# Kernel optimization log

Hardware: AMD Instinct MI355X
Metric: run time of the kernel (lower is better)

Reference implementation:

```python
import jax, jax.numpy as jnp
import numpy as np

B, S, D, H = 8, 1300, 1080, 12
DK = D // H  # 90
FF = 3 * D   # 3240
EPS = 1e-5


def _layernorm(x, g, b):
    m = jnp.mean(x, axis=-1, keepdims=True)
    v = jnp.var(x, axis=-1, keepdims=True)
    return (x - m) * jax.lax.rsqrt(v + EPS) * g + b


def _rotate_half(x):
    x1, x2 = jnp.split(x, 2, axis=-1)
    return jnp.concatenate([-x2, x1], axis=-1)


def _rope(x, cos, sin):
    # x: [B,H,S,DK]; cos/sin: [S,DK] broadcast over batch/heads
    return x * cos + _rotate_half(x) * sin


def setup_inputs() -> dict:
    key = jax.random.key(0)
    ks = jax.random.split(key, 20)
    w = lambda k, sh: jax.random.normal(k, sh, dtype=jnp.float32) * 0.02
    inp = {
        'x': jax.random.normal(ks[0], (B, S, D), dtype=jnp.float32),
        'mask': jnp.tril(jnp.ones((S, S), dtype=jnp.int32))[None, None, :, :],
        'Wq': w(ks[1], (D, D)), 'bq': jnp.zeros((D,), jnp.float32),
        'Wk': w(ks[2], (D, D)), 'bk': jnp.zeros((D,), jnp.float32),
        'Wv': w(ks[3], (D, D)), 'bv': jnp.zeros((D,), jnp.float32),
        'Wo': w(ks[4], (D, D)), 'bo': jnp.zeros((D,), jnp.float32),
        'W1': w(ks[5], (D, FF)), 'b1': jnp.zeros((FF,), jnp.float32),
        'W2': w(ks[6], (FF, D)), 'b2': jnp.zeros((D,), jnp.float32),
        'W3': w(ks[7], (D, FF)), 'b3': jnp.zeros((FF,), jnp.float32),
        'ln1_g': jnp.ones((D,), jnp.float32), 'ln1_b': jnp.zeros((D,), jnp.float32),
        'ln2_g': jnp.ones((D,), jnp.float32), 'ln2_b': jnp.zeros((D,), jnp.float32),
    }
    # RoPE tables (buffers, not trainable)
    inv_freq = 1.0 / (10000.0 ** (jnp.arange(0, DK, 2, dtype=jnp.float32) / DK))
    t = jnp.arange(S, dtype=jnp.float32)
    freqs = t[:, None] * inv_freq[None, :]          # [S, DK/2]
    emb = jnp.concatenate([freqs, freqs], axis=-1)  # [S, DK]
    inp['rope_cos'] = jnp.cos(emb)
    inp['rope_sin'] = jnp.sin(emb)
    return inp


def reference(x, mask, Wq, bq, Wk, bk, Wv, bv, Wo, bo,
              W1, b1, W2, b2, W3, b3, ln1_g, ln1_b, ln2_g, ln2_b,
              rope_cos, rope_sin):
    # pre-norm attention block
    x2 = _layernorm(x, ln1_g, ln1_b)
    q = (x2 @ Wq + bq).reshape(B, S, H, DK).transpose(0, 2, 1, 3)  # [B,H,S,DK]
    k = (x2 @ Wk + bk).reshape(B, S, H, DK).transpose(0, 2, 1, 3)
    v = (x2 @ Wv + bv).reshape(B, S, H, DK).transpose(0, 2, 1, 3)
    q = _rope(q, rope_cos, rope_sin)
    k = _rope(k, rope_cos, rope_sin)
    scores = jnp.einsum('bhqd,bhkd->bhqk', q, k) / jnp.sqrt(jnp.float32(DK))
    scores = jnp.where(mask == 0, jnp.float32(-1e9), scores)
    p = jax.nn.softmax(scores, axis=-1)
    attn = jnp.einsum('bhqk,bhkd->bhqd', p, v)
    attn = attn.transpose(0, 2, 1, 3).reshape(B, S, D)
    x = x + (attn @ Wo + bo)
    # pre-norm SwiGLU FFN block
    x2 = _layernorm(x, ln2_g, ln2_b)
    h = jax.nn.silu(x2 @ W1 + b1) * (x2 @ W3 + b3)
    x = x + (h @ W2 + b2)
    return x
```

## Files before the change

### kernel.cpp

```cpp
#include <hip/hip_runtime.h>
#include <hip/hip_bf16.h>
#include <cstdint>
#include <cstddef>

#define B_  8
#define S_  1300
#define D_  1080
#define H_  12
#define DK_ 90
#define FF_ 3240
#define MROWS (B_*S_)
#define KP1 1088
#define KP2 3264
#define SP  1312
#define QSCALE 0.105409255338946f

typedef __hip_bfloat16 bf16;
typedef __bf16 bf16x8 __attribute__((ext_vector_type(8)));
typedef float  f32x4  __attribute__((ext_vector_type(4)));
typedef unsigned short u16x8 __attribute__((ext_vector_type(8)));

__device__ __forceinline__ void gload16(const void* g, void* l) {
    __builtin_amdgcn_global_load_lds((const __attribute__((address_space(1))) void*)g,
                                     (__attribute__((address_space(3))) void*)l, 16, 0, 0);
}
__device__ __forceinline__ unsigned short bf16bits(float f) {
    bf16 b = __float2bfloat16(f);
    return *(unsigned short*)&b;
}

__global__ __launch_bounds__(256) void zero_pads(bf16* __restrict__ buf)
{
    const int idx = blockIdx.x * 256 + threadIdx.x;
    if (idx >= MROWS * (KP1 - D_)) return;
    const int row = idx >> 3, col = D_ + (idx & 7);
    buf[(size_t)row * KP1 + col] = __float2bfloat16(0.f);
}

__global__ __launch_bounds__(256) void castT(const float* __restrict__ W,
    bf16* __restrict__ WT, int K, int N, int KP)
{
    __shared__ unsigned short t[32][33];
    const int tx = threadIdx.x & 31, ty = threadIdx.x >> 5;
    const int k0 = blockIdx.x * 32, n0 = blockIdx.y * 32;
    #pragma unroll
    for (int i = 0; i < 4; ++i) {
        const int k = k0 + ty + 8 * i;
        const int n = n0 + tx;
        float v = (k < K && n < N) ? W[(size_t)k * N + n] : 0.f;
        t[ty + 8 * i][tx] = bf16bits(v);
    }
    __syncthreads();
    #pragma unroll
    for (int i = 0; i < 4; ++i) {
        const int n = n0 + ty + 8 * i;
        const int kk = k0 + tx;
        if (n < N && kk < KP) *(unsigned short*)&WT[(size_t)n * KP + kk] = t[tx][ty + 8 * i];
    }
}

__global__ __launch_bounds__(256) void ln_kernel(const float* __restrict__ x,
    const float* __restrict__ g, const float* __restrict__ b,
    bf16* __restrict__ y)
{
    __shared__ float xs[D_];
    __shared__ float red[8];
    const int row = blockIdx.x;
    const int tid = threadIdx.x;
    const float* xr = x + (size_t)row * D_;

    float s = 0.f, sq = 0.f;
    for (int d = tid; d < D_; d += 256) {
        float v = xr[d];
        xs[d] = v;
        s += v; sq += v * v;
    }
    #pragma unroll
    for (int off = 32; off > 0; off >>= 1) {
        s  += __shfl_down(s,  off, 64);
        sq += __shfl_down(sq, off, 64);
    }
    const int wave = tid >> 6, lane = tid & 63;
    if (lane == 0) { red[wave] = s; red[4 + wave] = sq; }
    __syncthreads();
    if (tid == 0) {
        float ts = 0.f, tq = 0.f;
        #pragma unroll
        for (int w = 0; w < 4; ++w) { ts += red[w]; tq += red[4 + w]; }
        red[0] = ts; red[4] = tq;
    }
    __syncthreads();
    const float mean = red[0] * (1.0f / D_);
    const float var  = red[4] * (1.0f / D_) - mean * mean;
    const float rstd = rsqrtf(var + 1e-5f);
    bf16* yr = y + (size_t)row * KP1;
    for (int d = tid; d < D_; d += 256)
        yr[d] = __float2bfloat16((xs[d] - mean) * rstd * g[d] + b[d]);
}

template<int MODE>
__global__ __launch_bounds__(256) void gemm_bf16(
    const bf16* __restrict__ A, const bf16* __restrict__ BT,
    const float* __restrict__ bias, const float* __restrict__ res,
    float* __restrict__ Cf, bf16* __restrict__ Cb,
    int M, int N, int KP, int LDC, int NP)
{
    __shared__ unsigned short As[128 * 32];
    __shared__ unsigned short Bs[128 * 32];

    const int tid = threadIdx.x;
    const int w = tid >> 6, l = tid & 63;
    const int m0 = blockIdx.y * 128, n0 = blockIdx.x * 128;

    const int rs = w * 16 + (l >> 2);
    const int kc = (l & 3) * 8;
    const int ar0 = min(m0 + rs,      M - 1);
    const int ar1 = min(m0 + rs + 64, M - 1);
    const int br0 = min(n0 + rs,      N - 1);
    const int br1 = min(n0 + rs + 64, N - 1);

    const int wm = (w >> 1) * 64, wn = (w & 1) * 64;
    const int lr = l & 15, kq = l >> 4;

    const unsigned short* aptr[4];
    const unsigned short* bptr[4];
    #pragma unroll
    for (int i = 0; i < 4; ++i) {
        aptr[i] = &As[(wm + i * 16 + lr) * 32 + kq * 8];
        bptr[i] = &Bs[(wn + i * 16 + lr) * 32 + kq * 8];
    }

    f32x4 acc[4][4] = {};

    const int nkt = KP >> 5;
    for (int kt = 0; kt < nkt; ++kt) {
        const int k0 = kt << 5;
        __syncthreads();
        gload16(A  + (size_t)ar0 * KP + k0 + kc, &As[w * 512]);
        gload16(A  + (size_t)ar1 * KP + k0 + kc, &As[2048 + w * 512]);
        gload16(BT + (size_t)br0 * KP + k0 + kc, &Bs[w * 512]);
        gload16(BT + (size_t)br1 * KP + k0 + kc, &Bs[2048 + w * 512]);
        __syncthreads();

        bf16x8 af[4], bv[4];
        #pragma unroll
        for (int i = 0; i < 4; ++i) af[i] = *(const bf16x8*)aptr[i];
        #pragma unroll
        for (int j = 0; j < 4; ++j) bv[j] = *(const bf16x8*)bptr[j];
        #pragma unroll
        for (int i = 0; i < 4; ++i)
            #pragma unroll
            for (int j = 0; j < 4; ++j)
                acc[i][j] = __builtin_amdgcn_mfma_f32_16x16x32_bf16(af[i], bv[j], acc[i][j], 0, 0, 0);
    }

    #pragma unroll
    for (int j = 0; j < 4; ++j) {
        const int n = n0 + wn + j * 16 + lr;
        if (n >= NP) continue;
        const bool real = (n < N);
        const float bn = real ? bias[n] : 0.f;
        #pragma unroll
        for (int i = 0; i < 4; ++i) {
            const int rowb = m0 + wm + i * 16 + kq * 4;
            #pragma unroll
            for (int r = 0; r < 4; ++r) {
                const int m = rowb + r;
                if (m < M) {
                    const size_t off = (size_t)m * LDC + n;
                    float val = acc[i][j][r] + bn;
                    if (MODE == 0) Cf[off] = val;
                    if (MODE == 1) Cf[off] = val + res[off];
                    if (MODE == 3) Cb[off] = real ? __float2bfloat16(val) : __float2bfloat16(0.f);
                    if (MODE == 2) {
                        if (real) {
                            const float prev = __bfloat162float(Cb[off]);
                            const float sig  = 1.0f / (1.0f + __expf(-prev));
                            Cb[off] = __float2bfloat16(prev * sig * val);
                        } else {
                            Cb[off] = __float2bfloat16(0.f);
                        }
                    }
                }
            }
        }
    }
}

__global__ __launch_bounds__(256) void rope_qk(const float* __restrict__ qb,
    const float* __restrict__ kb, const float* __restrict__ cosb,
    const float* __restrict__ sinb, bf16* __restrict__ Qa, bf16* __restrict__ Ka)
{
    const int s = blockIdx.x;
    const int b = blockIdx.y;
    const int tid = threadIdx.x;

    if (s >= S_) {
        for (int idx = tid; idx < H_ * 96; idx += 256) {
            const int h = idx / 96, c = idx - (idx / 96) * 96;
            const size_t o = ((size_t)(b * H_ + h) * SP + s) * 96 + c;
            Qa[o] = __float2bfloat16(0.f);
            Ka[o] = __float2bfloat16(0.f);
        }
        return;
    }

    const float* qr = qb + (size_t)(b * S_ + s) * D_;
    const float* kr = kb + (size_t)(b * S_ + s) * D_;

    for (int idx = tid; idx < H_ * 45; idx += 256) {
        const int h = idx / 45, d = idx - (idx / 45) * 45;
        const float c1 = cosb[s * DK_ + d],      s1 = sinb[s * DK_ + d];
        const float c2 = cosb[s * DK_ + d + 45], s2 = sinb[s * DK_ + d + 45];
        const size_t o = ((size_t)(b * H_ + h) * SP + s) * 96;
        const float q1 = qr[h * DK_ + d], q2 = qr[h * DK_ + d + 45];
        Qa[o + d]      = __float2bfloat16((q1 * c1 - q2 * s1) * QSCALE);
        Qa[o + d + 45] = __float2bfloat16((q2 * c2 + q1 * s2) * QSCALE);
        const float k1 = kr[h * DK_ + d], k2 = kr[h * DK_ + d + 45];
        Ka[o + d]      = __float2bfloat16(k1 * c1 - k2 * s1);
        Ka[o + d + 45] = __float2bfloat16(k2 * c2 + k1 * s2);
    }
    for (int idx = tid; idx < H_ * 6; idx += 256) {
        const int h = idx / 6, c = 90 + (idx - (idx / 6) * 6);
        const size_t o = ((size_t)(b * H_ + h) * SP + s) * 96 + c;
        Qa[o] = __float2bfloat16(0.f);
        Ka[o] = __float2bfloat16(0.f);
    }
}

__global__ __launch_bounds__(256) void vtrans(const float* __restrict__ vb,
    bf16* __restrict__ Vt)
{
    __shared__ float T[96][33];
    const int k0 = blockIdx.x * 32;
    const int bh = blockIdx.y;
    const int b = bh / H_, h = bh % H_;
    const int tid = threadIdx.x;

    for (int idx = tid; idx < 32 * 90; idx += 256) {
        const int r = idx / 90, d = idx - (idx / 90) * 90;
        const int s = k0 + r;
        T[d][r] = (s < S_) ? vb[(size_t)(b * S_ + s) * D_ + h * DK_ + d] : 0.f;
    }
    for (int idx = tid; idx < 32 * 6; idx += 256) {
        const int r = idx / 6, d = 90 + (idx - (idx / 6) * 6);
        T[d][r] = 0.f;
    }
    __syncthreads();
    for (int idx = tid; idx < 96 * 4; idx += 256) {
        const int d = idx >> 2, kk = (idx & 3) * 8;
        u16x8 v;
        #pragma unroll
        for (int i = 0; i < 8; ++i) v[i] = bf16bits(T[d][kk + i]);
        *(u16x8*)(Vt + ((size_t)bh * 96 + d) * SP + k0 + kk) = v;
    }
}

__global__ __launch_bounds__(256) void attn_mfma(const bf16* __restrict__ Qa,
    const bf16* __restrict__ Ka, const bf16* __restrict__ Vt,
    bf16* __restrict__ ab)
{
    __shared__ unsigned short Qs[64][104];
    __shared__ unsigned short Ks[32][104];
    __shared__ unsigned short Vs[96][40];
    __shared__ unsigned short Ps[4][16][40];

    const int tid = threadIdx.x;
    const int w = tid >> 6, l = tid & 63;
    const int lr = l & 15, kq = l >> 4;
    const int qblk = (int)gridDim.x - 1 - (int)blockIdx.x;
    const int q0 = qblk * 64;
    const int bh = blockIdx.y;
    const int b = bh / H_, h = bh % H_;

    const bf16* Qg = Qa + (size_t)bh * SP * 96;
    const bf16* Kg = Ka + (size_t)bh * SP * 96;
    const bf16* Vg = Vt + (size_t)bh * 96 * SP;

    for (int c = tid; c < 768; c += 256) {
        const int row = c / 12, cc = c - row * 12;
        const int rg = q0 + row;
        u16x8 v = (u16x8)0;
        if (rg < SP) v = *(const u16x8*)(Qg + (size_t)rg * 96 + cc * 8);
        *(u16x8*)&Qs[row][cc * 8] = v;
    }
    __syncthreads();

    bf16x8 Qf[3];
    #pragma unroll
    for (int kf = 0; kf < 3; ++kf)
        Qf[kf] = *(const bf16x8*)&Qs[w * 16 + lr][kf * 32 + kq * 8];

    const int qw0 = q0 + w * 16;
    const int wlq = (qw0 < S_) ? min(qw0 + 15, S_ - 1) : -1;
    const int lastq = min(q0 + 63, S_ - 1);
    const int ntiles = lastq / 32 + 1;

    f32x4 Of[6] = {};
    float mrun[4] = {-1e30f, -1e30f, -1e30f, -1e30f};
    float lrun[4] = {0.f, 0.f, 0.f, 0.f};

    for (int kt = 0; kt < ntiles; ++kt) {
        const int k0 = kt * 32;
        __syncthreads();
        for (int c = tid; c < 384; c += 256) {
            const int row = c / 12, cc = c - (c / 12) * 12;
            *(u16x8*)&Ks[row][cc * 8] = *(const u16x8*)(Kg + (size_t)(k0 + row) * 96 + cc * 8);
        }
        for (int c = tid; c < 384; c += 256) {
            const int d = c >> 2, kk = (c & 3) * 8;
            *(u16x8*)&Vs[d][kk] = *(const u16x8*)(Vg + (size_t)d * SP + k0 + kk);
        }
        __syncthreads();

        if (k0 > wlq) continue;

        f32x4 sg0 = {0.f, 0.f, 0.f, 0.f}, sg1 = {0.f, 0.f, 0.f, 0.f};
        #pragma unroll
        for (int kf = 0; kf < 3; ++kf) {
            bf16x8 k0f = *(const bf16x8*)&Ks[lr][kf * 32 + kq * 8];
            bf16x8 k1f = *(const bf16x8*)&Ks[16 + lr][kf * 32 + kq * 8];
            sg0 = __builtin_amdgcn_mfma_f32_16x16x32_bf16(Qf[kf], k0f, sg0, 0, 0, 0);
            sg1 = __builtin_amdgcn_mfma_f32_16x16x32_bf16(Qf[kf], k1f, sg1, 0, 0, 0);
        }

        const int key0 = k0 + lr, key1 = k0 + 16 + lr;
        float s0[4], s1[4], m4[4];
        #pragma unroll
        for (int r = 0; r < 4; ++r) {
            const int qrow = qw0 + 4 * kq + r;
            s0[r] = (key0 <= qrow && key0 < S_) ? sg0[r] : -1e30f;
            s1[r] = (key1 <= qrow && key1 < S_) ? sg1[r] : -1e30f;
            m4[r] = fmaxf(s0[r], s1[r]);
        }
        #pragma unroll
        for (int st = 1; st < 16; st <<= 1)
            #pragma unroll
            for (int r = 0; r < 4; ++r)
                m4[r] = fmaxf(m4[r], __shfl_xor(m4[r], st, 64));
        float resc[4], ls[4];
        #pragma unroll
        for (int r = 0; r < 4; ++r) {
            const float nm = fmaxf(mrun[r], m4[r]);
            resc[r] = __expf(mrun[r] - nm);
            mrun[r] = nm;
            const float e0 = (s0[r] > -1e29f) ? __expf(s0[r] - nm) : 0.f;
            const float e1 = (s1[r] > -1e29f) ? __expf(s1[r] - nm) : 0.f;
            Ps[w][4 * kq + r][lr]      = bf16bits(e0);
            Ps[w][4 * kq + r][16 + lr] = bf16bits(e1);
            ls[r] = e0 + e1;
        }
        #pragma unroll
        for (int st = 1; st < 16; st <<= 1)
            #pragma unroll
            for (int r = 0; r < 4; ++r)
                ls[r] += __shfl_xor(ls[r], st, 64);
        #pragma unroll
        for (int r = 0; r < 4; ++r) lrun[r] = lrun[r] * resc[r] + ls[r];
        #pragma unroll
        for (int c = 0; c < 6; ++c)
            #pragma unroll
            for (int r = 0; r < 4; ++r)
                Of[c][r] *= resc[r];

        bf16x8 Pf = *(const bf16x8*)&Ps[w][lr][kq * 8];
        #pragma unroll
        for (int c = 0; c < 6; ++c) {
            bf16x8 Vf = *(const bf16x8*)&Vs[16 * c + lr][kq * 8];
            Of[c] = __builtin_amdgcn_mfma_f32_16x16x32_bf16(Pf, Vf, Of[c], 0, 0, 0);
        }
    }

    float inv[4];
    #pragma unroll
    for (int r = 0; r < 4; ++r) inv[r] = 1.0f / lrun[r];
    #pragma unroll
    for (int c = 0; c < 6; ++c) {
        const int dim = 16 * c + lr;
        if (dim >= DK_) continue;
        #pragma unroll
        for (int r = 0; r < 4; ++r) {
            const int qrow = qw0 + 4 * kq + r;
            if (qrow < S_)
                ab[(size_t)(b * S_ + qrow) * KP1 + h * DK_ + dim] =
                    __float2bfloat16(Of[c][r] * inv[r]);
        }
    }
}

extern "C" void kernel_launch(void* const* d_in, const int* in_sizes, int n_in,
                              void* d_out, int out_size, void* d_ws, size_t ws_size,
                              hipStream_t stream)
{
    const float* x    = (const float*)d_in[0];
    const float* Wq   = (const float*)d_in[2];
    const float* bq   = (const float*)d_in[3];
    const float* Wk   = (const float*)d_in[4];
    const float* bk   = (const float*)d_in[5];
    const float* Wv   = (const float*)d_in[6];
    const float* bv   = (const float*)d_in[7];
    const float* Wo   = (const float*)d_in[8];
    const float* bo   = (const float*)d_in[9];
    const float* W1   = (const float*)d_in[10];
    const float* b1   = (const float*)d_in[11];
    const float* W2   = (const float*)d_in[12];
    const float* b2   = (const float*)d_in[13];
    const float* W3   = (const float*)d_in[14];
    const float* b3   = (const float*)d_in[15];
    const float* ln1g = (const float*)d_in[16];
    const float* ln1b = (const float*)d_in[17];
    const float* ln2g = (const float*)d_in[18];
    const float* ln2b = (const float*)d_in[19];
    const float* rc   = (const float*)d_in[20];
    const float* rs   = (const float*)d_in[21];
    float* out = (float*)d_out;

    char* wsb = (char*)d_ws;
    size_t off = 0;
    auto nxt = [&](size_t bytes) -> char* {
        char* p = wsb + off; off += (bytes + 255) & ~(size_t)255; return p;
    };
    bf16*  x2  = (bf16*)nxt((size_t)MROWS * KP1 * 2);
    float* qb  = (float*)nxt((size_t)MROWS * D_ * 4);
    float* kb  = (float*)nxt((size_t)MROWS * D_ * 4);
    float* vb  = (float*)nxt((size_t)MROWS * D_ * 4);
    bf16*  ab  = (bf16*)nxt((size_t)MROWS * KP1 * 2);
    bf16*  WqT = (bf16*)nxt((size_t)D_ * KP1 * 2);
    bf16*  WkT = (bf16*)nxt((size_t)D_ * KP1 * 2);
    bf16*  WvT = (bf16*)nxt((size_t)D_ * KP1 * 2);
    bf16*  WoT = (bf16*)nxt((size_t)D_ * KP1 * 2);
    bf16*  W1T = (bf16*)nxt((size_t)FF_ * KP1 * 2);
    bf16*  W3T = (bf16*)nxt((size_t)FF_ * KP1 * 2);
    bf16*  W2T = (bf16*)nxt((size_t)D_ * KP2 * 2);
    bf16*  Qa  = (bf16*)nxt((size_t)B_ * H_ * SP * 96 * 2);
    bf16*  Ka  = (bf16*)nxt((size_t)B_ * H_ * SP * 96 * 2);
    float* x1  = qb;
    bf16*  Vt  = (bf16*)kb;
    bf16*  hb  = (bf16*)kb;

    const dim3 blk(256);
    const dim3 gD(9, 82);
    const dim3 gF(26, 82);
    const int padN = MROWS * (KP1 - D_);

    zero_pads<<<(padN + 255) / 256, blk, 0, stream>>>(x2);
    zero_pads<<<(padN + 255) / 256, blk, 0, stream>>>(ab);

    castT<<<dim3(34, 34),  blk, 0, stream>>>(Wq, WqT, D_, D_, KP1);
    castT<<<dim3(34, 34),  blk, 0, stream>>>(Wk, WkT, D_, D_, KP1);
    castT<<<dim3(34, 34),  blk, 0, stream>>>(Wv, WvT, D_, D_, KP1);
    castT<<<dim3(34, 34),  blk, 0, stream>>>(Wo, WoT, D_, D_, KP1);
    castT<<<dim3(34, 102), blk, 0, stream>>>(W1, W1T, D_, FF_, KP1);
    castT<<<dim3(34, 102), blk, 0, stream>>>(W3, W3T, D_, FF_, KP1);
    castT<<<dim3(102, 34), blk, 0, stream>>>(W2, W2T, FF_, D_, KP2);

    ln_kernel<<<MROWS, blk, 0, stream>>>(x, ln1g, ln1b, x2);
    gemm_bf16<0><<<gD, blk, 0, stream>>>(x2, WqT, bq, nullptr, qb, nullptr, MROWS, D_, KP1, D_, D_);
    gemm_bf16<0><<<gD, blk, 0, stream>>>(x2, WkT, bk, nullptr, kb, nullptr, MROWS, D_, KP1, D_, D_);
    gemm_bf16<0><<<gD, blk, 0, stream>>>(x2, WvT, bv, nullptr, vb, nullptr, MROWS, D_, KP1, D_, D_);
    rope_qk<<<dim3(SP, B_), blk, 0, stream>>>(qb, kb, rc, rs, Qa, Ka);
    vtrans<<<dim3(41, B_ * H_), blk, 0, stream>>>(vb, Vt);
    attn_mfma<<<dim3(21, B_ * H_), blk, 0, stream>>>(Qa, Ka, Vt, ab);
    gemm_bf16<1><<<gD, blk, 0, stream>>>(ab, WoT, bo, x, x1, nullptr, MROWS, D_, KP1, D_, D_);
    ln_kernel<<<MROWS, blk, 0, stream>>>(x1, ln2g, ln2b, x2);
    gemm_bf16<3><<<gF, blk, 0, stream>>>(x2, W1T, b1, nullptr, nullptr, hb, MROWS, FF_, KP1, KP2, KP2);
    gemm_bf16<2><<<gF, blk, 0, stream>>>(x2, W3T, b3, nullptr, nullptr, hb, MROWS, FF_, KP1, KP2, KP2);
    gemm_bf16<1><<<gD, blk, 0, stream>>>(hb, W2T, b2, x1, out, nullptr, MROWS, D_, KP2, D_, D_);
}
```

Before: 1.235 ms.

## Fuse QKV projections into one bf16 GEMM and restructure attention softmax layout

Concatenates Wq/Wk/Wv and their biases so one GEMM (bf16 output mode) produces a combined QKV buffer, replacing three fp32-output GEMMs. RoPE and V-transpose read the bf16 buffer instead, which halves their intermediate traffic and shares the activation loads across all three projections. The attention kernel also swaps the MFMA operand order so each lane owns one query row, which reduces the softmax row reductions to two cross-lane shuffles and lets P be written with vector stores. The trade-off is that Q/K/V are rounded to bf16 before RoPE, which costs some precision.

```diff
diff --git a/kernel.cpp b/kernel.cpp
--- a/kernel.cpp
+++ b/kernel.cpp
@@ -13,6 +13,7 @@
 #define KP1 1088
 #define KP2 3264
 #define SP  1312
+#define QKVN 3240
 #define QSCALE 0.105409255338946f
 
 typedef __hip_bfloat16 bf16;
@@ -35,6 +36,15 @@
     if (idx >= MROWS * (KP1 - D_)) return;
     const int row = idx >> 3, col = D_ + (idx & 7);
     buf[(size_t)row * KP1 + col] = __float2bfloat16(0.f);
+}
+
+__global__ __launch_bounds__(256) void bcat(const float* __restrict__ bq,
+    const float* __restrict__ bk, const float* __restrict__ bv,
+    float* __restrict__ bqkv)
+{
+    const int i = blockIdx.x * 256 + threadIdx.x;
+    if (i >= QKVN) return;
+    bqkv[i] = (i < D_) ? bq[i] : (i < 2 * D_) ? bk[i - D_] : bv[i - 2 * D_];
 }
 
 __global__ __launch_bounds__(256) void castT(const float* __restrict__ W,
@@ -187,9 +197,9 @@
     }
 }
 
-__global__ __launch_bounds__(256) void rope_qk(const float* __restrict__ qb,
-    const float* __restrict__ kb, const float* __restrict__ cosb,
-    const float* __restrict__ sinb, bf16* __restrict__ Qa, bf16* __restrict__ Ka)
+__global__ __launch_bounds__(256) void rope_qk(const bf16* __restrict__ qkv,
+    const float* __restrict__ cosb, const float* __restrict__ sinb,
+    bf16* __restrict__ Qa, bf16* __restrict__ Ka)
 {
     const int s = blockIdx.x;
     const int b = blockIdx.y;
@@ -205,18 +215,19 @@
         return;
     }
 
-    const float* qr = qb + (size_t)(b * S_ + s) * D_;
-    const float* kr = kb + (size_t)(b * S_ + s) * D_;
+    const bf16* row = qkv + (size_t)(b * S_ + s) * QKVN;
 
     for (int idx = tid; idx < H_ * 45; idx += 256) {
         const int h = idx / 45, d = idx - (idx / 45) * 45;
         const float c1 = cosb[s * DK_ + d],      s1 = sinb[s * DK_ + d];
         const float c2 = cosb[s * DK_ + d + 45], s2 = sinb[s * DK_ + d + 45];
         const size_t o = ((size_t)(b * H_ + h) * SP + s) * 96;
-        const float q1 = qr[h * DK_ + d], q2 = qr[h * DK_ + d + 45];
+        const float q1 = __bfloat162float(row[h * DK_ + d]);
+        const float q2 = __bfloat162float(row[h * DK_ + d + 45]);
         Qa[o + d]      = __float2bfloat16((q1 * c1 - q2 * s1) * QSCALE);
         Qa[o + d + 45] = __float2bfloat16((q2 * c2 + q1 * s2) * QSCALE);
-        const float k1 = kr[h * DK_ + d], k2 = kr[h * DK_ + d + 45];
+        const float k1 = __bfloat162float(row[D_ + h * DK_ + d]);
+        const float k2 = __bfloat162float(row[D_ + h * DK_ + d + 45]);
         Ka[o + d]      = __float2bfloat16(k1 * c1 - k2 * s1);
         Ka[o + d + 45] = __float2bfloat16(k2 * c2 + k1 * s2);
     }
@@ -228,7 +239,7 @@
     }
 }
 
-__global__ __launch_bounds__(256) void vtrans(const float* __restrict__ vb,
+__global__ __launch_bounds__(256) void vtrans(const bf16* __restrict__ qkv,
     bf16* __restrict__ Vt)
 {
     __shared__ float T[96][33];
@@ -240,7 +251,8 @@
     for (int idx = tid; idx < 32 * 90; idx += 256) {
         const int r = idx / 90, d = idx - (idx / 90) * 90;
         const int s = k0 + r;
-        T[d][r] = (s < S_) ? vb[(size_t)(b * S_ + s) * D_ + h * DK_ + d] : 0.f;
+        T[d][r] = (s < S_) ?
+            __bfloat162float(qkv[(size_t)(b * S_ + s) * QKVN + 2 * D_ + h * DK_ + d]) : 0.f;
     }
     for (int idx = tid; idx < 32 * 6; idx += 256) {
         const int r = idx / 6, d = 90 + (idx - (idx / 6) * 6);
@@ -292,13 +304,13 @@
         Qf[kf] = *(const bf16x8*)&Qs[w * 16 + lr][kf * 32 + kq * 8];
 
     const int qw0 = q0 + w * 16;
+    const int myq = qw0 + lr;
     const int wlq = (qw0 < S_) ? min(qw0 + 15, S_ - 1) : -1;
     const int lastq = min(q0 + 63, S_ - 1);
     const int ntiles = lastq / 32 + 1;
 
     f32x4 Of[6] = {};
-    float mrun[4] = {-1e30f, -1e30f, -1e30f, -1e30f};
-    float lrun[4] = {0.f, 0.f, 0.f, 0.f};
+    float mrun = -1e30f, lrun = 0.f;
 
     for (int kt = 0; kt < ntiles; ++kt) {
         const int k0 = kt * 32;
@@ -320,48 +332,50 @@
         for (int kf = 0; kf < 3; ++kf) {
             bf16x8 k0f = *(const bf16x8*)&Ks[lr][kf * 32 + kq * 8];
             bf16x8 k1f = *(const bf16x8*)&Ks[16 + lr][kf * 32 + kq * 8];
-            sg0 = __builtin_amdgcn_mfma_f32_16x16x32_bf16(Qf[kf], k0f, sg0, 0, 0, 0);
-            sg1 = __builtin_amdgcn_mfma_f32_16x16x32_bf16(Qf[kf], k1f, sg1, 0, 0, 0);
-        }
-
-        const int key0 = k0 + lr, key1 = k0 + 16 + lr;
-        float s0[4], s1[4], m4[4];
+            sg0 = __builtin_amdgcn_mfma_f32_16x16x32_bf16(k0f, Qf[kf], sg0, 0, 0, 0);
+            sg1 = __builtin_amdgcn_mfma_f32_16x16x32_bf16(k1f, Qf[kf], sg1, 0, 0, 0);
+        }
+
+        float e[8];
+        float msub = -1e30f;
         #pragma unroll
         for (int r = 0; r < 4; ++r) {
-            const int qrow = qw0 + 4 * kq + r;
-            s0[r] = (key0 <= qrow && key0 < S_) ? sg0[r] : -1e30f;
-            s1[r] = (key1 <= qrow && key1 < S_) ? sg1[r] : -1e30f;
-            m4[r] = fmaxf(s0[r], s1[r]);
-        }
-        #pragma unroll
-        for (int st = 1; st < 16; st <<= 1)
-            #pragma unroll
-            for (int r = 0; r < 4; ++r)
-                m4[r] = fmaxf(m4[r], __shfl_xor(m4[r], st, 64));
-        float resc[4], ls[4];
-        #pragma unroll
-        for (int r = 0; r < 4; ++r) {
-            const float nm = fmaxf(mrun[r], m4[r]);
-            resc[r] = __expf(mrun[r] - nm);
-            mrun[r] = nm;
-            const float e0 = (s0[r] > -1e29f) ? __expf(s0[r] - nm) : 0.f;
-            const float e1 = (s1[r] > -1e29f) ? __expf(s1[r] - nm) : 0.f;
-            Ps[w][4 * kq + r][lr]      = bf16bits(e0);
-            Ps[w][4 * kq + r][16 + lr] = bf16bits(e1);
-            ls[r] = e0 + e1;
-        }
-        #pragma unroll
-        for (int st = 1; st < 16; st <<= 1)
-            #pragma unroll
-            for (int r = 0; r < 4; ++r)
-                ls[r] += __shfl_xor(ls[r], st, 64);
-        #pragma unroll
-        for (int r = 0; r < 4; ++r) lrun[r] = lrun[r] * resc[r] + ls[r];
+            const int ka = k0 + 4 * kq + r;
+            const int kb = ka + 16;
+            const float a = (ka <= myq && ka < S_) ? sg0[r] : -1e30f;
+            const float c = (kb <= myq && kb < S_) ? sg1[r] : -1e30f;
+            e[r] = a; e[4 + r] = c;
+            msub = fmaxf(msub, fmaxf(a, c));
+        }
+        msub = fmaxf(msub, __shfl_xor(msub, 16, 64));
+        msub = fmaxf(msub, __shfl_xor(msub, 32, 64));
+        const float nm = fmaxf(mrun, msub);
+        const float resc = __expf(mrun - nm);
+        mrun = nm;
+        float ls = 0.f;
+        #pragma unroll
+        for (int i = 0; i < 8; ++i) {
+            const float ev = (e[i] > -1e29f) ? __expf(e[i] - nm) : 0.f;
+            e[i] = ev; ls += ev;
+        }
+        ls += __shfl_xor(ls, 16, 64);
+        ls += __shfl_xor(ls, 32, 64);
+        lrun = lrun * resc + ls;
+
+        ushort4 p0, p1;
+        p0.x = bf16bits(e[0]); p0.y = bf16bits(e[1]); p0.z = bf16bits(e[2]); p0.w = bf16bits(e[3]);
+        p1.x = bf16bits(e[4]); p1.y = bf16bits(e[5]); p1.z = bf16bits(e[6]); p1.w = bf16bits(e[7]);
+        *(ushort4*)&Ps[w][lr][4 * kq]      = p0;
+        *(ushort4*)&Ps[w][lr][16 + 4 * kq] = p1;
+
+        float rf[4];
+        #pragma unroll
+        for (int r = 0; r < 4; ++r) rf[r] = __shfl(resc, 4 * kq + r, 16);
         #pragma unroll
         for (int c = 0; c < 6; ++c)
             #pragma unroll
             for (int r = 0; r < 4; ++r)
-                Of[c][r] *= resc[r];
+                Of[c][r] *= rf[r];
 
         bf16x8 Pf = *(const bf16x8*)&Ps[w][lr][kq * 8];
         #pragma unroll
@@ -371,9 +385,10 @@
         }
     }
 
+    const float invq = 1.0f / lrun;
     float inv[4];
     #pragma unroll
-    for (int r = 0; r < 4; ++r) inv[r] = 1.0f / lrun[r];
+    for (int r = 0; r < 4; ++r) inv[r] = __shfl(invq, 4 * kq + r, 16);
     #pragma unroll
     for (int c = 0; c < 6; ++c) {
         const int dim = 16 * c + lr;
@@ -420,23 +435,21 @@
     auto nxt = [&](size_t bytes) -> char* {
         char* p = wsb + off; off += (bytes + 255) & ~(size_t)255; return p;
     };
-    bf16*  x2  = (bf16*)nxt((size_t)MROWS * KP1 * 2);
-    float* qb  = (float*)nxt((size_t)MROWS * D_ * 4);
-    float* kb  = (float*)nxt((size_t)MROWS * D_ * 4);
-    float* vb  = (float*)nxt((size_t)MROWS * D_ * 4);
-    bf16*  ab  = (bf16*)nxt((size_t)MROWS * KP1 * 2);
-    bf16*  WqT = (bf16*)nxt((size_t)D_ * KP1 * 2);
-    bf16*  WkT = (bf16*)nxt((size_t)D_ * KP1 * 2);
-    bf16*  WvT = (bf16*)nxt((size_t)D_ * KP1 * 2);
-    bf16*  WoT = (bf16*)nxt((size_t)D_ * KP1 * 2);
-    bf16*  W1T = (bf16*)nxt((size_t)FF_ * KP1 * 2);
-    bf16*  W3T = (bf16*)nxt((size_t)FF_ * KP1 * 2);
-    bf16*  W2T = (bf16*)nxt((size_t)D_ * KP2 * 2);
-    bf16*  Qa  = (bf16*)nxt((size_t)B_ * H_ * SP * 96 * 2);
-    bf16*  Ka  = (bf16*)nxt((size_t)B_ * H_ * SP * 96 * 2);
-    float* x1  = qb;
-    bf16*  Vt  = (bf16*)kb;
-    bf16*  hb  = (bf16*)kb;
+    bf16*  x2   = (bf16*)nxt((size_t)MROWS * KP1 * 2);
+    bf16*  qkv  = (bf16*)nxt((size_t)MROWS * KP2 * 2);
+    float* x1f  = (float*)nxt((size_t)MROWS * D_ * 4);
+    bf16*  ab   = (bf16*)nxt((size_t)MROWS * KP1 * 2);
+    bf16*  WqkvT= (bf16*)nxt((size_t)QKVN * KP1 * 2);
+    bf16*  WoT  = (bf16*)nxt((size_t)D_ * KP1 * 2);
+    bf16*  W1T  = (bf16*)nxt((size_t)FF_ * KP1 * 2);
+    bf16*  W3T  = (bf16*)nxt((size_t)FF_ * KP1 * 2);
+    bf16*  W2T  = (bf16*)nxt((size_t)D_ * KP2 * 2);
+    bf16*  Qa   = (bf16*)nxt((size_t)B_ * H_ * SP * 96 * 2);
+    bf16*  Ka   = (bf16*)nxt((size_t)B_ * H_ * SP * 96 * 2);
+    float* bqkv = (float*)nxt((size_t)QKVN * 4);
+    bf16*  Vt   = (bf16*)x1f;
+    float* x1   = x1f;
+    bf16*  hb   = qkv;
 
     const dim3 blk(256);
     const dim3 gD(9, 82);
@@ -445,21 +458,21 @@
 
     zero_pads<<<(padN + 255) / 256, blk, 0, stream>>>(x2);
     zero_pads<<<(padN + 255) / 256, blk, 0, stream>>>(ab);
-
-    castT<<<dim3(34, 34),  blk, 0, stream>>>(Wq, WqT, D_, D_, KP1);
-    castT<<<dim3(34, 34),  blk, 0, stream>>>(Wk, WkT, D_, D_, KP1);
-    castT<<<dim3(34, 34),  blk, 0, stream>>>(Wv, WvT, D_, D_, KP1);
+    bcat<<<(QKVN + 255) / 256, blk, 0, stream>>>(bq, bk, bv, bqkv);
+
+    castT<<<dim3(34, 34),  blk, 0, stream>>>(Wq, WqkvT,                    D_, D_, KP1);
+    castT<<<dim3(34, 34),  blk, 0, stream>>>(Wk, WqkvT + (size_t)D_ * KP1, D_, D_, KP1);
+    castT<<<dim3(34, 34),  blk, 0, stream>>>(Wv, WqkvT + (size_t)2*D_*KP1, D_, D_, KP1);
     castT<<<dim3(34, 34),  blk, 0, stream>>>(Wo, WoT, D_, D_, KP1);
     castT<<<dim3(34, 102), blk, 0, stream>>>(W1, W1T, D_, FF_, KP1);
     castT<<<dim3(34, 102), blk, 0, stream>>>(W3, W3T, D_, FF_, KP1);
     castT<<<dim3(102, 34), blk, 0, stream>>>(W2, W2T, FF_, D_, KP2);
 
     ln_kernel<<<MROWS, blk, 0, stream>>>(x, ln1g, ln1b, x2);
-    gemm_bf16<0><<<gD, blk, 0, stream>>>(x2, WqT, bq, nullptr, qb, nullptr, MROWS, D_, KP1, D_, D_);
-    gemm_bf16<0><<<gD, blk, 0, stream>>>(x2, WkT, bk, nullptr, kb, nullptr, MROWS, D_, KP1, D_, D_);
-    gemm_bf16<0><<<gD, blk, 0, stream>>>(x2, WvT, bv, nullptr, vb, nullptr, MROWS, D_, KP1, D_, D_);
-    rope_qk<<<dim3(SP, B_), blk, 0, stream>>>(qb, kb, rc, rs, Qa, Ka);
-    vtrans<<<dim3(41, B_ * H_), blk, 0, stream>>>(vb, Vt);
+    gemm_bf16<3><<<gF, blk, 0, stream>>>(x2, WqkvT, bqkv, nullptr, nullptr, qkv,
+                                         MROWS, QKVN, KP1, QKVN, QKVN);
+    rope_qk<<<dim3(SP, B_), blk, 0, stream>>>(qkv, rc, rs, Qa, Ka);
+    vtrans<<<dim3(41, B_ * H_), blk, 0, stream>>>(qkv, Vt);
     attn_mfma<<<dim3(21, B_ * H_), blk, 0, stream>>>(Qa, Ka, Vt, ab);
     gemm_bf16<1><<<gD, blk, 0, stream>>>(ab, WoT, bo, x, x1, nullptr, MROWS, D_, KP1, D_, D_);
     ln_kernel<<<MROWS, blk, 0, stream>>>(x1, ln2g, ln2b, x2);
```

New measurement: 1.147 ms. -7.1%, faster.
